# Performance work log

Measured on AMD Instinct MI355X. Metric: run time of the kernel, lower is better.

Reference implementation:

```python
import jax, jax.numpy as jnp
import numpy as np

C = 768            # config.channels
CH, CW = 16, 16    # coarse span shape for group 'screen'
N = CH * CW        # total coarse positions = 256
FH, FW, FP = 16, 16, 2
F = FH * FW * FP   # fine_total = 512
K = 4              # top4 sample mode
B = 1024           # sb


def _ln(x, g, b, eps=1e-5):
    m = jnp.mean(x, axis=-1, keepdims=True)
    v = jnp.mean((x - m) ** 2, axis=-1, keepdims=True)
    return (x - m) / jnp.sqrt(v + eps) * g + b


def _mlp3(x, W1, b1, W2, b2, W3, b3):
    h = jax.nn.gelu(x @ W1 + b1)
    h = jax.nn.gelu(h @ W2 + b2)
    return h @ W3 + b3


def setup_inputs() -> dict:
    key = jax.random.key(0)
    ks = jax.random.split(key, 16)

    def w(k, fan_in, shape):
        return jax.random.normal(k, shape, jnp.float32) * (1.0 / np.sqrt(fan_in))

    return {
        "x": jax.random.normal(ks[0], (B, C), jnp.float32),
        "g_in": jnp.ones((C,), jnp.float32),
        "b_in": jnp.zeros((C,), jnp.float32),
        # coarse head: C -> C -> C -> N
        "cW1": w(ks[1], C, (C, C)), "cb1": jnp.zeros((C,), jnp.float32),
        "cW2": w(ks[2], C, (C, C)), "cb2": jnp.zeros((C,), jnp.float32),
        "cW3": w(ks[3], C, (C, N)), "cb3": jnp.zeros((N,), jnp.float32),
        # coarse embedding
        "emb": jax.random.normal(ks[4], (N, C), jnp.float32),
        "g_e": jnp.ones((C,), jnp.float32),
        "b_e": jnp.zeros((C,), jnp.float32),
        # fine head: 2C -> C -> C -> F
        "fW1": w(ks[5], 2 * C, (2 * C, C)), "fb1": jnp.zeros((C,), jnp.float32),
        "fW2": w(ks[6], C, (C, C)), "fb2": jnp.zeros((C,), jnp.float32),
        "fW3": w(ks[7], C, (C, F)), "fb3": jnp.zeros((F,), jnp.float32),
        # no-op head
        "nW": w(ks[8], C, (C, 1)), "nb": jnp.zeros((1,), jnp.float32),
    }


def reference(x, g_in, b_in, cW1, cb1, cW2, cb2, cW3, cb3, emb, g_e, b_e,
              fW1, fb1, fW2, fb2, fW3, fb3, nW, nb):
    b = x.shape[0]
    xn = _ln(x, g_in, b_in)                                   # (b, C)
    no_op = xn @ nW + nb                                      # (b, 1)
    coarse = _mlp3(xn, cW1, cb1, cW2, cb2, cW3, cb3)          # (b, N)

    # top4 routing
    _, i = jax.lax.top_k(coarse, K)                           # (b, K) int32
    e = _ln(emb[i], g_e, b_e)                                 # (b, K, C)
    fine_in = jnp.concatenate(
        [jnp.broadcast_to(xn[:, None, :], (b, K, C)), e], axis=-1)  # (b, K, 2C)
    fine = _mlp3(fine_in, fW1, fb1, fW2, fb2, fW3, fb3)       # (b, K, F)

    log_f = jnp.log(jnp.float32(F))
    xfull = jnp.broadcast_to(coarse[:, :, None], (b, N, F)) - log_f  # (b, N, F)
    upd = fine + log_f - jax.nn.logsumexp(fine, axis=-1, keepdims=True)
    xfull = xfull.at[jnp.arange(b)[:, None], i].add(upd)      # scatter-combine

    # per-group permute: (b, ch, cw, fh, fw, fp) -> (b, ch, fh, cw, fw, fp)
    xg = xfull.reshape(b, CH, CW, FH, FW, FP)
    xg = jnp.transpose(xg, (0, 1, 3, 2, 4, 5)).reshape(b, -1)
    return jnp.concatenate([no_op, xg], axis=-1)              # (b, 1 + N*F)
```

## Files before the change

### kernel.cpp

```cpp
#include <hip/hip_runtime.h>
#include <hip/hip_bf16.h>
#include <math.h>

typedef unsigned short u16;
typedef unsigned int   u32;
typedef __attribute__((ext_vector_type(8))) short s16x8;
typedef __attribute__((ext_vector_type(4))) float f32x4;

#define CB 768
#define NB 256
#define FB 512
#define BATCH 1024
#define OUTC 131073
#define LOGF 6.2383246250395077f

#define OFF_X    0
#define OFF_GIN  786432
#define OFF_BIN  787200
#define OFF_CW1  787968
#define OFF_CB1  1377792
#define OFF_CW2  1378560
#define OFF_CB2  1968384
#define OFF_CW3  1969152
#define OFF_CB3  2165760
#define OFF_EMB  2166016
#define OFF_GE   2362624
#define OFF_BE   2363392
#define OFF_FW1  2364160
#define OFF_FB1  3543808
#define OFF_FW2  3544576
#define OFF_FB2  4134400
#define OFF_FW3  4135168
#define OFF_FB3  4528384
#define OFF_NW   4528896
#define OFF_NB   4529664
#define MASTER_TOTAL 4529665

struct Ptrs20 { const void* p[20]; };

__device__ __forceinline__ u16 f2bf(float f){
    u32 u = __float_as_uint(f);
    u32 r = u + 0x7FFFu + ((u >> 16) & 1u);
    return (u16)(r >> 16);
}
__device__ __forceinline__ float bf2f(u16 s){ return __uint_as_float(((u32)s) << 16); }

__device__ __forceinline__ float gelu_f(float x){
    return 0.5f * x * (1.0f + tanhf(0.7978845608028654f * (x + 0.044715f * x * x * x)));
}

__device__ __forceinline__ f32x4 mfma16x16x32(s16x8 a, s16x8 b, f32x4 c){
    return __builtin_amdgcn_mfma_f32_16x16x32_bf16(a, b, c, 0, 0, 0);
}

__device__ __forceinline__ float blockReduce(float v, float* sb, bool domax){
    #pragma unroll
    for (int o = 32; o > 0; o >>= 1){
        float ov = __shfl_down(v, o, 64);
        v = domax ? fmaxf(v, ov) : (v + ov);
    }
    int w = threadIdx.x >> 6, lane = threadIdx.x & 63;
    if (lane == 0) sb[w] = v;
    __syncthreads();
    float r = domax ? fmaxf(fmaxf(sb[0], sb[1]), fmaxf(sb[2], sb[3]))
                    : (sb[0] + sb[1] + sb[2] + sb[3]);
    __syncthreads();
    return r;
}

__global__ __launch_bounds__(256) void convert_k(Ptrs20 ip, float* __restrict__ m){
    const int SZ[20]  = {786432,768,768,589824,768,589824,768,196608,256,196608,
                         768,768,1179648,768,589824,768,393216,512,768,1};
    const int OFF[20] = {OFF_X,OFF_GIN,OFF_BIN,OFF_CW1,OFF_CB1,OFF_CW2,OFF_CB2,OFF_CW3,OFF_CB3,OFF_EMB,
                         OFF_GE,OFF_BE,OFF_FW1,OFF_FB1,OFF_FW2,OFF_FB2,OFF_FW3,OFF_FB3,OFF_NW,OFF_NB};
    int t = blockIdx.y;
    int n = SZ[t];
    int i0 = (blockIdx.x * 256 + threadIdx.x) * 4;
    if (i0 >= n) return;
    bool isbf = (((const u16*)ip.p[1])[0] == 0x3F80u);
    float* dst = m + OFF[t] + i0;
    if (isbf){
        const u16* s = (const u16*)ip.p[t] + i0;
        #pragma unroll
        for (int e = 0; e < 4; e++) if (i0 + e < n) dst[e] = bf2f(s[e]);
    } else {
        const float* s = (const float*)ip.p[t] + i0;
        #pragma unroll
        for (int e = 0; e < 4; e++) if (i0 + e < n) dst[e] = s[e];
    }
}

template<int SPL>
__global__ __launch_bounds__(256) void transpose_k(const float* __restrict__ W,
        u16* __restrict__ Wh, u16* __restrict__ Wl, int K, int N){
    __shared__ float t[32][33];
    int n0 = blockIdx.x * 32, k0 = blockIdx.y * 32;
    int tx = threadIdx.x & 31, ty = threadIdx.x >> 5;
    #pragma unroll
    for (int i = 0; i < 32; i += 8)
        t[ty + i][tx] = W[(size_t)(k0 + ty + i) * N + n0 + tx];
    __syncthreads();
    #pragma unroll
    for (int i = 0; i < 32; i += 8){
        float f = t[tx][ty + i];
        u16 h = f2bf(f);
        Wh[(size_t)(n0 + ty + i) * K + k0 + tx] = h;
        if (SPL == 2)
            Wl[(size_t)(n0 + ty + i) * K + k0 + tx] = f2bf(f - bf2f(h));
    }
}

__global__ __launch_bounds__(256) void ln_x_k(const float* __restrict__ x,
        const float* __restrict__ g, const float* __restrict__ bb,
        const float* __restrict__ nW, const float* __restrict__ nb,
        float* __restrict__ xn_f32, u16* __restrict__ xn_bf, float* __restrict__ noop){
    __shared__ float sb[4];
    int b = blockIdx.x, tid = threadIdx.x;
    const float* xr = x + (size_t)b * CB;
    float v[3];
    #pragma unroll
    for (int i = 0; i < 3; i++) v[i] = xr[tid + i * 256];
    float mean = blockReduce(v[0] + v[1] + v[2], sb, false) * (1.0f / 768.0f);
    float d0 = v[0] - mean, d1 = v[1] - mean, d2 = v[2] - mean;
    float var = blockReduce(d0*d0 + d1*d1 + d2*d2, sb, false) * (1.0f / 768.0f);
    float inv = 1.0f / sqrtf(var + 1e-5f);
    float dot = 0.0f;
    #pragma unroll
    for (int i = 0; i < 3; i++){
        int c = tid + i * 256;
        float xi = (v[i] - mean) * inv * g[c] + bb[c];
        xn_f32[(size_t)b * CB + c] = xi;
        xn_bf[(size_t)b * CB + c] = f2bf(xi);
        dot += xi * nW[c];
    }
    dot = blockReduce(dot, sb, false);
    if (tid == 0) noop[b] = dot + nb[0];
}

template<int ASPLIT, int BSPLIT, int ACT, int OUTBF>
__global__ __launch_bounds__(256) void gemm_k(const void* __restrict__ Ap,
        const u16* __restrict__ Bth, const u16* __restrict__ Btl,
        const float* __restrict__ bias, void* __restrict__ Outp, int M, int N, int K){
    constexpr int LDA = 40;
    __shared__ u16 As[ASPLIT][128 * LDA];
    __shared__ u16 Bs[BSPLIT][64 * LDA];
    const int m0 = blockIdx.y * 128, n0 = blockIdx.x * 64;
    const int tid = threadIdx.x;
    const int w = tid >> 6, lane = tid & 63, lm = lane & 15, q = lane >> 4;
    f32x4 acc[2][4];
    #pragma unroll
    for (int i = 0; i < 2; i++)
        #pragma unroll
        for (int j = 0; j < 4; j++) acc[i][j] = (f32x4)(0.0f);
    const int ar = tid >> 1, ac = (tid & 1) * 16;
    const int bn = tid >> 2, bc = (tid & 3) * 8;

    for (int k0 = 0; k0 < K; k0 += 32){
        __syncthreads();
        if (ASPLIT == 3){
            const float* src = (const float*)Ap + (size_t)(m0 + ar) * K + k0 + ac;
            short hi[16], lo[16], l2[16];
            #pragma unroll
            for (int h = 0; h < 4; h++){
                float4 vv = ((const float4*)src)[h];
                float e4[4] = {vv.x, vv.y, vv.z, vv.w};
                #pragma unroll
                for (int e = 0; e < 4; e++){
                    float f = e4[e];
                    u16 hb = f2bf(f);  float fh = bf2f(hb);
                    float r1 = f - fh; u16 lb = f2bf(r1); float fl = bf2f(lb);
                    float r2 = r1 - fl; u16 qb = f2bf(r2);
                    hi[h*4+e] = (short)hb; lo[h*4+e] = (short)lb; l2[h*4+e] = (short)qb;
                }
            }
            *(s16x8*)&As[0][ar*LDA + ac]     = *(s16x8*)&hi[0];
            *(s16x8*)&As[0][ar*LDA + ac + 8] = *(s16x8*)&hi[8];
            *(s16x8*)&As[1][ar*LDA + ac]     = *(s16x8*)&lo[0];
            *(s16x8*)&As[1][ar*LDA + ac + 8] = *(s16x8*)&lo[8];
            *(s16x8*)&As[2][ar*LDA + ac]     = *(s16x8*)&l2[0];
            *(s16x8*)&As[2][ar*LDA + ac + 8] = *(s16x8*)&l2[8];
        } else {
            const u16* src = (const u16*)Ap + (size_t)(m0 + ar) * K + k0 + ac;
            *(s16x8*)&As[0][ar*LDA + ac]     = *(const s16x8*)(src);
            *(s16x8*)&As[0][ar*LDA + ac + 8] = *(const s16x8*)(src + 8);
        }
        *(s16x8*)&Bs[0][bn*LDA + bc] = *(const s16x8*)(Bth + (size_t)(n0 + bn) * K + k0 + bc);
        if (BSPLIT == 2)
            *(s16x8*)&Bs[1][bn*LDA + bc] = *(const s16x8*)(Btl + (size_t)(n0 + bn) * K + k0 + bc);
        __syncthreads();

        s16x8 afr[ASPLIT][2], bfr[BSPLIT][4];
        #pragma unroll
        for (int mt = 0; mt < 2; mt++)
            #pragma unroll
            for (int s = 0; s < ASPLIT; s++)
                afr[s][mt] = *(const s16x8*)&As[s][(w*32 + mt*16 + lm)*LDA + q*8];
        #pragma unroll
        for (int nt = 0; nt < 4; nt++)
            #pragma unroll
            for (int s = 0; s < BSPLIT; s++)
                bfr[s][nt] = *(const s16x8*)&Bs[s][(nt*16 + lm)*LDA + q*8];
        #pragma unroll
        for (int mt = 0; mt < 2; mt++)
            #pragma unroll
            for (int nt = 0; nt < 4; nt++){
                acc[mt][nt] = mfma16x16x32(afr[0][mt], bfr[0][nt], acc[mt][nt]);
                if (ASPLIT == 3){
                    acc[mt][nt] = mfma16x16x32(afr[1][mt], bfr[0][nt], acc[mt][nt]);
                    acc[mt][nt] = mfma16x16x32(afr[2][mt], bfr[0][nt], acc[mt][nt]);
                }
                if (BSPLIT == 2){
                    acc[mt][nt] = mfma16x16x32(afr[0][mt], bfr[1][nt], acc[mt][nt]);
                    if (ASPLIT == 3)
                        acc[mt][nt] = mfma16x16x32(afr[1][mt], bfr[1][nt], acc[mt][nt]);
                }
            }
    }
    #pragma unroll
    for (int nt = 0; nt < 4; nt++){
        int n = n0 + nt*16 + lm;
        float bv = bias[n];
        #pragma unroll
        for (int mt = 0; mt < 2; mt++){
            #pragma unroll
            for (int r = 0; r < 4; r++){
                int m = m0 + w*32 + mt*16 + q*4 + r;
                float vv = acc[mt][nt][r] + bv;
                if (ACT == 1) vv = gelu_f(vv);
                if (OUTBF) ((u16*)Outp)[(size_t)m * N + n] = f2bf(vv);
                else       ((float*)Outp)[(size_t)m * N + n] = vv;
            }
        }
    }
}

__global__ __launch_bounds__(64) void topk_k(const float* __restrict__ coarse,
        int* __restrict__ idx, unsigned char* __restrict__ ksel){
    int b = blockIdx.x, lane = threadIdx.x;
    const float* cr = coarse + (size_t)b * NB;
    float v[4]; int id[4];
    #pragma unroll
    for (int j = 0; j < 4; j++){ id[j] = lane + 64*j; v[j] = cr[id[j]]; }
    ((u32*)(ksel + (size_t)b * NB))[lane] = 0xFFFFFFFFu;
    __syncthreads();
    for (int k = 0; k < 4; k++){
        float bv = v[0]; int bi = id[0];
        #pragma unroll
        for (int j = 1; j < 4; j++)
            if (v[j] > bv || (v[j] == bv && id[j] < bi)){ bv = v[j]; bi = id[j]; }
        #pragma unroll
        for (int o = 32; o > 0; o >>= 1){
            float ov = __shfl_xor(bv, o, 64);
            int   oi = __shfl_xor(bi, o, 64);
            if (ov > bv || (ov == bv && oi < bi)){ bv = ov; bi = oi; }
        }
        if (lane == 0){ idx[b*4 + k] = bi; ksel[(size_t)b * NB + bi] = (unsigned char)k; }
        #pragma unroll
        for (int j = 0; j < 4; j++) if (id[j] == bi) v[j] = -INFINITY;
    }
}

__global__ __launch_bounds__(256) void finein_k(const int* __restrict__ idx,
        const float* __restrict__ emb, const float* __restrict__ ge, const float* __restrict__ be,
        const u16* __restrict__ xnb, u16* __restrict__ fin){
    __shared__ float sb[4];
    int bk = blockIdx.x, tid = threadIdx.x;
    int b = bk >> 2;
    int n = idx[bk];
    const float* er = emb + (size_t)n * CB;
    float v[3];
    #pragma unroll
    for (int i = 0; i < 3; i++) v[i] = er[tid + i * 256];
    float mean = blockReduce(v[0] + v[1] + v[2], sb, false) * (1.0f / 768.0f);
    float d0 = v[0] - mean, d1 = v[1] - mean, d2 = v[2] - mean;
    float var = blockReduce(d0*d0 + d1*d1 + d2*d2, sb, false) * (1.0f / 768.0f);
    float inv = 1.0f / sqrtf(var + 1e-5f);
    u16* dst = fin + (size_t)bk * (2 * CB);
    #pragma unroll
    for (int i = 0; i < 3; i++){
        int c = tid + i * 256;
        dst[c] = xnb[(size_t)b * CB + c];
        dst[CB + c] = f2bf((v[i] - mean) * inv * ge[c] + be[c]);
    }
}

__global__ __launch_bounds__(256) void upd_k(float* __restrict__ fine){
    __shared__ float sb[4];
    int bk = blockIdx.x, tid = threadIdx.x;
    float* fr = fine + (size_t)bk * FB;
    float a = fr[tid], b2 = fr[tid + 256];
    float mx = blockReduce(fmaxf(a, b2), sb, true);
    float es = expf(a - mx) + expf(b2 - mx);
    float ssum = blockReduce(es, sb, false);
    float off = LOGF - (mx + logf(ssum));
    fr[tid] = a + off;
    fr[tid + 256] = b2 + off;
}

__global__ __launch_bounds__(256) void out_k(const float* __restrict__ coarse,
        const float* __restrict__ upd, const unsigned char* __restrict__ ksel,
        const float* __restrict__ noop, const void* __restrict__ g_in_raw,
        void* __restrict__ outp){
    u32 g0 = ((u32)blockIdx.x * 256u + (u32)threadIdx.x) * 8u;
    const u32 total = (u32)BATCH * (u32)OUTC;
    if (g0 >= total) return;
    bool isbf = (((const u16*)g_in_raw)[0] == 0x3F80u);
    float vals[8];
    #pragma unroll
    for (int e = 0; e < 8; e++){
        u32 gg = g0 + (u32)e;
        u32 qq = gg >> 17;
        int rr = (int)(gg & 131071u) - (int)qq;
        if (rr < 0){ qq -= 1u; rr += 131073; }
        int b = (int)qq;
        float val;
        if (rr == 0){
            val = noop[b];
        } else {
            int j = rr - 1;
            int ch = j >> 13;
            int rem = j & 8191;
            int fh = rem >> 9, cw = (rem >> 5) & 15, ff = rem & 31;
            int n = (ch << 4) + cw;
            val = coarse[(size_t)b * NB + n] - LOGF;
            int ks = ksel[(size_t)b * NB + n];
            if (ks != 255) val += upd[(((size_t)b * 4 + ks) << 9) + (fh << 5) + ff];
        }
        vals[e] = val;
    }
    if (isbf){
        u16 res[8];
        #pragma unroll
        for (int e = 0; e < 8; e++) res[e] = f2bf(vals[e]);
        *(s16x8*)((u16*)outp + g0) = *(s16x8*)res;
    } else {
        float* of = (float*)outp + g0;
        *(float4*)(of)     = make_float4(vals[0], vals[1], vals[2], vals[3]);
        *(float4*)(of + 4) = make_float4(vals[4], vals[5], vals[6], vals[7]);
    }
}

extern "C" void kernel_launch(void* const* d_in, const int* in_sizes, int n_in,
                              void* d_out, int out_size, void* d_ws, size_t ws_size,
                              hipStream_t stream){
    (void)in_sizes; (void)n_in; (void)out_size; (void)ws_size;
    char* ws = (char*)d_ws;
    size_t off = 0;
    auto alloc = [&](size_t bytes){ void* p = ws + off; off += (bytes + 255) & ~(size_t)255; return p; };

    float* master = (float*)alloc((size_t)MASTER_TOTAL * 4);
    u16*   xn_bf  = (u16*)  alloc((size_t)1024*768*2);
    u16*   fin    = (u16*)  alloc((size_t)4096*1536*2);
    float* fine   = (float*)alloc((size_t)4096*512*4);
    u16*   gg1    = (u16*)  alloc((size_t)4096*768*2);
    u16*   gg2    = (u16*)  alloc((size_t)4096*768*2);
    float* coarse = (float*)alloc((size_t)1024*256*4);
    int*   idx    = (int*)  alloc((size_t)1024*4*4);
    unsigned char* ksel = (unsigned char*)alloc((size_t)1024*256);
    float* noop   = (float*)alloc((size_t)1024*4);
    u16* cW1th = (u16*)alloc((size_t)768*768*2);
    u16* cW1tl = (u16*)alloc((size_t)768*768*2);
    u16* cW2th = (u16*)alloc((size_t)768*768*2);
    u16* cW2tl = (u16*)alloc((size_t)768*768*2);
    u16* cW3th = (u16*)alloc((size_t)768*256*2);
    u16* cW3tl = (u16*)alloc((size_t)768*256*2);
    u16* fW1t  = (u16*)alloc((size_t)1536*768*2);
    u16* fW2t  = (u16*)alloc((size_t)768*768*2);
    u16* fW3t  = (u16*)alloc((size_t)768*512*2);

    float* xn_f32 = (float*)fin;
    float* h1     = (float*)fine;
    float* h2     = (float*)gg1;

    Ptrs20 ip;
    for (int i = 0; i < 20; i++) ip.p[i] = d_in[i];

    convert_k<<<dim3(1152, 20), 256, 0, stream>>>(ip, master);

    transpose_k<2><<<dim3(24, 24), 256, 0, stream>>>(master + OFF_CW1, cW1th, cW1tl, 768, 768);
    transpose_k<2><<<dim3(24, 24), 256, 0, stream>>>(master + OFF_CW2, cW2th, cW2tl, 768, 768);
    transpose_k<2><<<dim3( 8, 24), 256, 0, stream>>>(master + OFF_CW3, cW3th, cW3tl, 768, 256);
    transpose_k<1><<<dim3(24, 48), 256, 0, stream>>>(master + OFF_FW1, fW1t, nullptr, 1536, 768);
    transpose_k<1><<<dim3(24, 24), 256, 0, stream>>>(master + OFF_FW2, fW2t, nullptr, 768, 768);
    transpose_k<1><<<dim3(16, 24), 256, 0, stream>>>(master + OFF_FW3, fW3t, nullptr, 768, 512);

    ln_x_k<<<1024, 256, 0, stream>>>(master + OFF_X, master + OFF_GIN, master + OFF_BIN,
                                     master + OFF_NW, master + OFF_NB, xn_f32, xn_bf, noop);

    gemm_k<3,2,1,0><<<dim3(12, 8), 256, 0, stream>>>(xn_f32, cW1th, cW1tl, master + OFF_CB1, h1, 1024, 768, 768);
    gemm_k<3,2,1,0><<<dim3(12, 8), 256, 0, stream>>>(h1,     cW2th, cW2tl, master + OFF_CB2, h2, 1024, 768, 768);
    gemm_k<3,2,0,0><<<dim3( 4, 8), 256, 0, stream>>>(h2,     cW3th, cW3tl, master + OFF_CB3, coarse, 1024, 256, 768);

    topk_k<<<1024, 64, 0, stream>>>(coarse, idx, ksel);
    finein_k<<<4096, 256, 0, stream>>>(idx, master + OFF_EMB, master + OFF_GE, master + OFF_BE, xn_bf, fin);

    gemm_k<1,1,1,1><<<dim3(12, 32), 256, 0, stream>>>(fin, fW1t, nullptr, master + OFF_FB1, gg1, 4096, 768, 1536);
    gemm_k<1,1,1,1><<<dim3(12, 32), 256, 0, stream>>>(gg1, fW2t, nullptr, master + OFF_FB2, gg2, 4096, 768, 768);
    gemm_k<1,1,0,0><<<dim3( 8, 32), 256, 0, stream>>>(gg2, fW3t, nullptr, master + OFF_FB3, fine, 4096, 512, 768);

    upd_k<<<4096, 256, 0, stream>>>(fine);

    u32 total_chunks = ((u32)BATCH * (u32)OUTC) / 8u;
    u32 blocks = (total_chunks + 255u) / 256u;
    out_k<<<blocks, 256, 0, stream>>>(coarse, fine, ksel, noop, d_in[1], d_out);
}
```

Baseline: 874.1 us.

## Drop fp32 staging copy, merge transposes, presplit activations, fuse softmax offset into output

Removes the convert kernel that copied all inputs into an fp32 master buffer; kernels now read the raw inputs directly and detect the dtype per load. The six weight transposes are merged into one launch driven by a descriptor table. Coarse-head activations are split into three bf16 parts once, in the producing kernel's epilogue, instead of being re-split inside every GEMM tile load. The in-place logsumexp update pass is replaced by a per-row offset kernel whose offset is added inside the output kernel. This cuts launches and redundant traffic and conversion work, at the cost of more intermediate buffers and three-way stores from the GEMM epilogue.

```diff
diff --git a/kernel.cpp b/kernel.cpp
--- a/kernel.cpp
+++ b/kernel.cpp
@@ -14,41 +14,24 @@
 #define OUTC 131073
 #define LOGF 6.2383246250395077f
 
-#define OFF_X    0
-#define OFF_GIN  786432
-#define OFF_BIN  787200
-#define OFF_CW1  787968
-#define OFF_CB1  1377792
-#define OFF_CW2  1378560
-#define OFF_CB2  1968384
-#define OFF_CW3  1969152
-#define OFF_CB3  2165760
-#define OFF_EMB  2166016
-#define OFF_GE   2362624
-#define OFF_BE   2363392
-#define OFF_FW1  2364160
-#define OFF_FB1  3543808
-#define OFF_FW2  3544576
-#define OFF_FB2  4134400
-#define OFF_FW3  4135168
-#define OFF_FB3  4528384
-#define OFF_NW   4528896
-#define OFF_NB   4529664
-#define MASTER_TOTAL 4529665
-
-struct Ptrs20 { const void* p[20]; };
-
 __device__ __forceinline__ u16 f2bf(float f){
     u32 u = __float_as_uint(f);
     u32 r = u + 0x7FFFu + ((u >> 16) & 1u);
     return (u16)(r >> 16);
 }
 __device__ __forceinline__ float bf2f(u16 s){ return __uint_as_float(((u32)s) << 16); }
-
+__device__ __forceinline__ bool probe_bf(const void* g){ return ((const u16*)g)[0] == 0x3F80u; }
+__device__ __forceinline__ float loadraw(const void* p, size_t i, bool isbf){
+    return isbf ? bf2f(((const u16*)p)[i]) : ((const float*)p)[i];
+}
+__device__ __forceinline__ void split3(float f, u16& h, u16& l, u16& q){
+    h = f2bf(f); float r1 = f - bf2f(h);
+    l = f2bf(r1); float r2 = r1 - bf2f(l);
+    q = f2bf(r2);
+}
 __device__ __forceinline__ float gelu_f(float x){
     return 0.5f * x * (1.0f + tanhf(0.7978845608028654f * (x + 0.044715f * x * x * x)));
 }
-
 __device__ __forceinline__ f32x4 mfma16x16x32(s16x8 a, s16x8 b, f32x4 c){
     return __builtin_amdgcn_mfma_f32_16x16x32_bf16(a, b, c, 0, 0, 0);
 }
@@ -68,58 +51,45 @@
     return r;
 }
 
-__global__ __launch_bounds__(256) void convert_k(Ptrs20 ip, float* __restrict__ m){
-    const int SZ[20]  = {786432,768,768,589824,768,589824,768,196608,256,196608,
-                         768,768,1179648,768,589824,768,393216,512,768,1};
-    const int OFF[20] = {OFF_X,OFF_GIN,OFF_BIN,OFF_CW1,OFF_CB1,OFF_CW2,OFF_CB2,OFF_CW3,OFF_CB3,OFF_EMB,
-                         OFF_GE,OFF_BE,OFF_FW1,OFF_FB1,OFF_FW2,OFF_FB2,OFF_FW3,OFF_FB3,OFF_NW,OFF_NB};
-    int t = blockIdx.y;
-    int n = SZ[t];
-    int i0 = (blockIdx.x * 256 + threadIdx.x) * 4;
-    if (i0 >= n) return;
-    bool isbf = (((const u16*)ip.p[1])[0] == 0x3F80u);
-    float* dst = m + OFF[t] + i0;
-    if (isbf){
-        const u16* s = (const u16*)ip.p[t] + i0;
-        #pragma unroll
-        for (int e = 0; e < 4; e++) if (i0 + e < n) dst[e] = bf2f(s[e]);
-    } else {
-        const float* s = (const float*)ip.p[t] + i0;
-        #pragma unroll
-        for (int e = 0; e < 4; e++) if (i0 + e < n) dst[e] = s[e];
-    }
-}
-
-template<int SPL>
-__global__ __launch_bounds__(256) void transpose_k(const float* __restrict__ W,
-        u16* __restrict__ Wh, u16* __restrict__ Wl, int K, int N){
+struct TransDesc { const void* src; u16* dh; u16* dl; int K; int N; int start; int tilesX; };
+struct TD6 { TransDesc d[6]; };
+
+__global__ __launch_bounds__(256) void transpose_all_k(TD6 td, const void* ginp){
+    bool isbf = probe_bf(ginp);
+    int blk = blockIdx.x;
+    int e = 0;
+    #pragma unroll
+    for (int i = 1; i < 6; i++) if (blk >= td.d[i].start) e = i;
+    TransDesc d = td.d[e];
+    int rel = blk - d.start;
+    int n0 = (rel % d.tilesX) * 32;
+    int k0 = (rel / d.tilesX) * 32;
     __shared__ float t[32][33];
-    int n0 = blockIdx.x * 32, k0 = blockIdx.y * 32;
     int tx = threadIdx.x & 31, ty = threadIdx.x >> 5;
     #pragma unroll
     for (int i = 0; i < 32; i += 8)
-        t[ty + i][tx] = W[(size_t)(k0 + ty + i) * N + n0 + tx];
+        t[ty + i][tx] = loadraw(d.src, (size_t)(k0 + ty + i) * d.N + n0 + tx, isbf);
     __syncthreads();
     #pragma unroll
     for (int i = 0; i < 32; i += 8){
         float f = t[tx][ty + i];
         u16 h = f2bf(f);
-        Wh[(size_t)(n0 + ty + i) * K + k0 + tx] = h;
-        if (SPL == 2)
-            Wl[(size_t)(n0 + ty + i) * K + k0 + tx] = f2bf(f - bf2f(h));
-    }
-}
-
-__global__ __launch_bounds__(256) void ln_x_k(const float* __restrict__ x,
-        const float* __restrict__ g, const float* __restrict__ bb,
-        const float* __restrict__ nW, const float* __restrict__ nb,
-        float* __restrict__ xn_f32, u16* __restrict__ xn_bf, float* __restrict__ noop){
+        d.dh[(size_t)(n0 + ty + i) * d.K + k0 + tx] = h;
+        if (d.dl)
+            d.dl[(size_t)(n0 + ty + i) * d.K + k0 + tx] = f2bf(f - bf2f(h));
+    }
+}
+
+__global__ __launch_bounds__(256) void ln_x_k(const void* x, const void* g, const void* bb,
+        const void* nW, const void* nb, const void* ginp,
+        u16* __restrict__ xh, u16* __restrict__ xl, u16* __restrict__ xq,
+        float* __restrict__ noop){
     __shared__ float sb[4];
+    bool isbf = probe_bf(ginp);
     int b = blockIdx.x, tid = threadIdx.x;
-    const float* xr = x + (size_t)b * CB;
     float v[3];
     #pragma unroll
-    for (int i = 0; i < 3; i++) v[i] = xr[tid + i * 256];
+    for (int i = 0; i < 3; i++) v[i] = loadraw(x, (size_t)b * CB + tid + i * 256, isbf);
     float mean = blockReduce(v[0] + v[1] + v[2], sb, false) * (1.0f / 768.0f);
     float d0 = v[0] - mean, d1 = v[1] - mean, d2 = v[2] - mean;
     float var = blockReduce(d0*d0 + d1*d1 + d2*d2, sb, false) * (1.0f / 768.0f);
@@ -128,22 +98,27 @@
     #pragma unroll
     for (int i = 0; i < 3; i++){
         int c = tid + i * 256;
-        float xi = (v[i] - mean) * inv * g[c] + bb[c];
-        xn_f32[(size_t)b * CB + c] = xi;
-        xn_bf[(size_t)b * CB + c] = f2bf(xi);
-        dot += xi * nW[c];
+        float xi = (v[i] - mean) * inv * loadraw(g, c, isbf) + loadraw(bb, c, isbf);
+        u16 h, l, q; split3(xi, h, l, q);
+        size_t o = (size_t)b * CB + c;
+        xh[o] = h; xl[o] = l; xq[o] = q;
+        dot += xi * loadraw(nW, c, isbf);
     }
     dot = blockReduce(dot, sb, false);
-    if (tid == 0) noop[b] = dot + nb[0];
-}
-
-template<int ASPLIT, int BSPLIT, int ACT, int OUTBF>
-__global__ __launch_bounds__(256) void gemm_k(const void* __restrict__ Ap,
+    if (tid == 0) noop[b] = dot + loadraw(nb, 0, isbf);
+}
+
+template<int ASPLIT, int BSPLIT, int ACT, int OUTMODE>
+__global__ __launch_bounds__(256) void gemm_k(
+        const u16* __restrict__ Ah, const u16* __restrict__ Al, const u16* __restrict__ Aq,
         const u16* __restrict__ Bth, const u16* __restrict__ Btl,
-        const float* __restrict__ bias, void* __restrict__ Outp, int M, int N, int K){
+        const void* __restrict__ bias, const void* __restrict__ ginp,
+        void* __restrict__ o0, void* __restrict__ o1, void* __restrict__ o2,
+        int M, int N, int K){
     constexpr int LDA = 40;
     __shared__ u16 As[ASPLIT][128 * LDA];
     __shared__ u16 Bs[BSPLIT][64 * LDA];
+    bool isbf = probe_bf(ginp);
     const int m0 = blockIdx.y * 128, n0 = blockIdx.x * 64;
     const int tid = threadIdx.x;
     const int w = tid >> 6, lane = tid & 63, lm = lane & 15, q = lane >> 4;
@@ -157,32 +132,18 @@
 
     for (int k0 = 0; k0 < K; k0 += 32){
         __syncthreads();
-        if (ASPLIT == 3){
-            const float* src = (const float*)Ap + (size_t)(m0 + ar) * K + k0 + ac;
-            short hi[16], lo[16], l2[16];
-            #pragma unroll
-            for (int h = 0; h < 4; h++){
-                float4 vv = ((const float4*)src)[h];
-                float e4[4] = {vv.x, vv.y, vv.z, vv.w};
-                #pragma unroll
-                for (int e = 0; e < 4; e++){
-                    float f = e4[e];
-                    u16 hb = f2bf(f);  float fh = bf2f(hb);
-                    float r1 = f - fh; u16 lb = f2bf(r1); float fl = bf2f(lb);
-                    float r2 = r1 - fl; u16 qb = f2bf(r2);
-                    hi[h*4+e] = (short)hb; lo[h*4+e] = (short)lb; l2[h*4+e] = (short)qb;
-                }
+        {
+            const u16* s0 = Ah + (size_t)(m0 + ar) * K + k0 + ac;
+            *(s16x8*)&As[0][ar*LDA + ac]     = *(const s16x8*)(s0);
+            *(s16x8*)&As[0][ar*LDA + ac + 8] = *(const s16x8*)(s0 + 8);
+            if (ASPLIT == 3){
+                const u16* s1 = Al + (size_t)(m0 + ar) * K + k0 + ac;
+                *(s16x8*)&As[1][ar*LDA + ac]     = *(const s16x8*)(s1);
+                *(s16x8*)&As[1][ar*LDA + ac + 8] = *(const s16x8*)(s1 + 8);
+                const u16* s2 = Aq + (size_t)(m0 + ar) * K + k0 + ac;
+                *(s16x8*)&As[2][ar*LDA + ac]     = *(const s16x8*)(s2);
+                *(s16x8*)&As[2][ar*LDA + ac + 8] = *(const s16x8*)(s2 + 8);
             }
-            *(s16x8*)&As[0][ar*LDA + ac]     = *(s16x8*)&hi[0];
-            *(s16x8*)&As[0][ar*LDA + ac + 8] = *(s16x8*)&hi[8];
-            *(s16x8*)&As[1][ar*LDA + ac]     = *(s16x8*)&lo[0];
-            *(s16x8*)&As[1][ar*LDA + ac + 8] = *(s16x8*)&lo[8];
-            *(s16x8*)&As[2][ar*LDA + ac]     = *(s16x8*)&l2[0];
-            *(s16x8*)&As[2][ar*LDA + ac + 8] = *(s16x8*)&l2[8];
-        } else {
-            const u16* src = (const u16*)Ap + (size_t)(m0 + ar) * K + k0 + ac;
-            *(s16x8*)&As[0][ar*LDA + ac]     = *(const s16x8*)(src);
-            *(s16x8*)&As[0][ar*LDA + ac + 8] = *(const s16x8*)(src + 8);
         }
         *(s16x8*)&Bs[0][bn*LDA + bc] = *(const s16x8*)(Bth + (size_t)(n0 + bn) * K + k0 + bc);
         if (BSPLIT == 2)
@@ -219,7 +180,7 @@
     #pragma unroll
     for (int nt = 0; nt < 4; nt++){
         int n = n0 + nt*16 + lm;
-        float bv = bias[n];
+        float bv = loadraw(bias, n, isbf);
         #pragma unroll
         for (int mt = 0; mt < 2; mt++){
             #pragma unroll
@@ -227,8 +188,13 @@
                 int m = m0 + w*32 + mt*16 + q*4 + r;
                 float vv = acc[mt][nt][r] + bv;
                 if (ACT == 1) vv = gelu_f(vv);
-                if (OUTBF) ((u16*)Outp)[(size_t)m * N + n] = f2bf(vv);
-                else       ((float*)Outp)[(size_t)m * N + n] = vv;
+                size_t o = (size_t)m * N + n;
+                if (OUTMODE == 0)      ((float*)o0)[o] = vv;
+                else if (OUTMODE == 1) ((u16*)o0)[o] = f2bf(vv);
+                else {
+                    u16 h, l, qq; split3(vv, h, l, qq);
+                    ((u16*)o0)[o] = h; ((u16*)o1)[o] = l; ((u16*)o2)[o] = qq;
+                }
             }
         }
     }
@@ -261,16 +227,16 @@
 }
 
 __global__ __launch_bounds__(256) void finein_k(const int* __restrict__ idx,
-        const float* __restrict__ emb, const float* __restrict__ ge, const float* __restrict__ be,
-        const u16* __restrict__ xnb, u16* __restrict__ fin){
+        const void* __restrict__ emb, const void* __restrict__ ge, const void* __restrict__ be,
+        const void* __restrict__ ginp, const u16* __restrict__ xh, u16* __restrict__ fin){
     __shared__ float sb[4];
+    bool isbf = probe_bf(ginp);
     int bk = blockIdx.x, tid = threadIdx.x;
     int b = bk >> 2;
     int n = idx[bk];
-    const float* er = emb + (size_t)n * CB;
     float v[3];
     #pragma unroll
-    for (int i = 0; i < 3; i++) v[i] = er[tid + i * 256];
+    for (int i = 0; i < 3; i++) v[i] = loadraw(emb, (size_t)n * CB + tid + i * 256, isbf);
     float mean = blockReduce(v[0] + v[1] + v[2], sb, false) * (1.0f / 768.0f);
     float d0 = v[0] - mean, d1 = v[1] - mean, d2 = v[2] - mean;
     float var = blockReduce(d0*d0 + d1*d1 + d2*d2, sb, false) * (1.0f / 768.0f);
@@ -279,32 +245,40 @@
     #pragma unroll
     for (int i = 0; i < 3; i++){
         int c = tid + i * 256;
-        dst[c] = xnb[(size_t)b * CB + c];
-        dst[CB + c] = f2bf((v[i] - mean) * inv * ge[c] + be[c]);
-    }
-}
-
-__global__ __launch_bounds__(256) void upd_k(float* __restrict__ fine){
-    __shared__ float sb[4];
-    int bk = blockIdx.x, tid = threadIdx.x;
-    float* fr = fine + (size_t)bk * FB;
-    float a = fr[tid], b2 = fr[tid + 256];
-    float mx = blockReduce(fmaxf(a, b2), sb, true);
-    float es = expf(a - mx) + expf(b2 - mx);
-    float ssum = blockReduce(es, sb, false);
-    float off = LOGF - (mx + logf(ssum));
-    fr[tid] = a + off;
-    fr[tid + 256] = b2 + off;
+        dst[c] = xh[(size_t)b * CB + c];
+        dst[CB + c] = f2bf((v[i] - mean) * inv * loadraw(ge, c, isbf) + loadraw(be, c, isbf));
+    }
+}
+
+__global__ __launch_bounds__(256) void updoff_k(const float* __restrict__ fine,
+        float* __restrict__ offs){
+    int row = blockIdx.x * 4 + (threadIdx.x >> 6);
+    int lane = threadIdx.x & 63;
+    const float* fr = fine + (size_t)row * FB;
+    float v[8];
+    #pragma unroll
+    for (int j = 0; j < 8; j++) v[j] = fr[lane + 64*j];
+    float mx = v[0];
+    #pragma unroll
+    for (int j = 1; j < 8; j++) mx = fmaxf(mx, v[j]);
+    #pragma unroll
+    for (int o = 32; o > 0; o >>= 1) mx = fmaxf(mx, __shfl_xor(mx, o, 64));
+    float es = 0.0f;
+    #pragma unroll
+    for (int j = 0; j < 8; j++) es += expf(v[j] - mx);
+    #pragma unroll
+    for (int o = 32; o > 0; o >>= 1) es += __shfl_xor(es, o, 64);
+    if (lane == 0) offs[row] = LOGF - (mx + logf(es));
 }
 
 __global__ __launch_bounds__(256) void out_k(const float* __restrict__ coarse,
-        const float* __restrict__ upd, const unsigned char* __restrict__ ksel,
-        const float* __restrict__ noop, const void* __restrict__ g_in_raw,
-        void* __restrict__ outp){
+        const float* __restrict__ fine, const float* __restrict__ offs,
+        const unsigned char* __restrict__ ksel, const float* __restrict__ noop,
+        const void* __restrict__ ginp, void* __restrict__ outp){
     u32 g0 = ((u32)blockIdx.x * 256u + (u32)threadIdx.x) * 8u;
     const u32 total = (u32)BATCH * (u32)OUTC;
     if (g0 >= total) return;
-    bool isbf = (((const u16*)g_in_raw)[0] == 0x3F80u);
+    bool isbf = probe_bf(ginp);
     float vals[8];
     #pragma unroll
     for (int e = 0; e < 8; e++){
@@ -324,7 +298,10 @@
             int n = (ch << 4) + cw;
             val = coarse[(size_t)b * NB + n] - LOGF;
             int ks = ksel[(size_t)b * NB + n];
-            if (ks != 255) val += upd[(((size_t)b * 4 + ks) << 9) + (fh << 5) + ff];
+            if (ks != 255){
+                int fr = b * 4 + ks;
+                val += fine[((size_t)fr << 9) + (fh << 5) + ff] + offs[fr];
+            }
         }
         vals[e] = val;
     }
@@ -348,16 +325,24 @@
     size_t off = 0;
     auto alloc = [&](size_t bytes){ void* p = ws + off; off += (bytes + 255) & ~(size_t)255; return p; };
 
-    float* master = (float*)alloc((size_t)MASTER_TOTAL * 4);
-    u16*   xn_bf  = (u16*)  alloc((size_t)1024*768*2);
-    u16*   fin    = (u16*)  alloc((size_t)4096*1536*2);
-    float* fine   = (float*)alloc((size_t)4096*512*4);
-    u16*   gg1    = (u16*)  alloc((size_t)4096*768*2);
-    u16*   gg2    = (u16*)  alloc((size_t)4096*768*2);
+    u16* xh  = (u16*)alloc((size_t)1024*768*2);
+    u16* xl  = (u16*)alloc((size_t)1024*768*2);
+    u16* xq  = (u16*)alloc((size_t)1024*768*2);
+    u16* h1h = (u16*)alloc((size_t)1024*768*2);
+    u16* h1l = (u16*)alloc((size_t)1024*768*2);
+    u16* h1q = (u16*)alloc((size_t)1024*768*2);
+    u16* h2h = (u16*)alloc((size_t)1024*768*2);
+    u16* h2l = (u16*)alloc((size_t)1024*768*2);
+    u16* h2q = (u16*)alloc((size_t)1024*768*2);
     float* coarse = (float*)alloc((size_t)1024*256*4);
     int*   idx    = (int*)  alloc((size_t)1024*4*4);
     unsigned char* ksel = (unsigned char*)alloc((size_t)1024*256);
     float* noop   = (float*)alloc((size_t)1024*4);
+    float* offs   = (float*)alloc((size_t)4096*4);
+    u16*   fin    = (u16*)  alloc((size_t)4096*1536*2);
+    u16*   gg1    = (u16*)  alloc((size_t)4096*768*2);
+    u16*   gg2    = (u16*)  alloc((size_t)4096*768*2);
+    float* fine   = (float*)alloc((size_t)4096*512*4);
     u16* cW1th = (u16*)alloc((size_t)768*768*2);
     u16* cW1tl = (u16*)alloc((size_t)768*768*2);
     u16* cW2th = (u16*)alloc((size_t)768*768*2);
@@ -368,39 +353,40 @@
     u16* fW2t  = (u16*)alloc((size_t)768*768*2);
     u16* fW3t  = (u16*)alloc((size_t)768*512*2);
 
-    float* xn_f32 = (float*)fin;
-    float* h1     = (float*)fine;
-    float* h2     = (float*)gg1;
-
-    Ptrs20 ip;
-    for (int i = 0; i < 20; i++) ip.p[i] = d_in[i];
-
-    convert_k<<<dim3(1152, 20), 256, 0, stream>>>(ip, master);
-
-    transpose_k<2><<<dim3(24, 24), 256, 0, stream>>>(master + OFF_CW1, cW1th, cW1tl, 768, 768);
-    transpose_k<2><<<dim3(24, 24), 256, 0, stream>>>(master + OFF_CW2, cW2th, cW2tl, 768, 768);
-    transpose_k<2><<<dim3( 8, 24), 256, 0, stream>>>(master + OFF_CW3, cW3th, cW3tl, 768, 256);
-    transpose_k<1><<<dim3(24, 48), 256, 0, stream>>>(master + OFF_FW1, fW1t, nullptr, 1536, 768);
-    transpose_k<1><<<dim3(24, 24), 256, 0, stream>>>(master + OFF_FW2, fW2t, nullptr, 768, 768);
-    transpose_k<1><<<dim3(16, 24), 256, 0, stream>>>(master + OFF_FW3, fW3t, nullptr, 768, 512);
-
-    ln_x_k<<<1024, 256, 0, stream>>>(master + OFF_X, master + OFF_GIN, master + OFF_BIN,
-                                     master + OFF_NW, master + OFF_NB, xn_f32, xn_bf, noop);
-
-    gemm_k<3,2,1,0><<<dim3(12, 8), 256, 0, stream>>>(xn_f32, cW1th, cW1tl, master + OFF_CB1, h1, 1024, 768, 768);
-    gemm_k<3,2,1,0><<<dim3(12, 8), 256, 0, stream>>>(h1,     cW2th, cW2tl, master + OFF_CB2, h2, 1024, 768, 768);
-    gemm_k<3,2,0,0><<<dim3( 4, 8), 256, 0, stream>>>(h2,     cW3th, cW3tl, master + OFF_CB3, coarse, 1024, 256, 768);
+    const void* ginp = d_in[1];
+
+    TD6 td;
+    td.d[0] = { d_in[3],  cW1th, cW1tl,  768, 768,    0, 24 };
+    td.d[1] = { d_in[5],  cW2th, cW2tl,  768, 768,  576, 24 };
+    td.d[2] = { d_in[7],  cW3th, cW3tl,  768, 256, 1152,  8 };
+    td.d[3] = { d_in[12], fW1t,  nullptr,1536, 768, 1344, 24 };
+    td.d[4] = { d_in[14], fW2t,  nullptr, 768, 768, 2496, 24 };
+    td.d[5] = { d_in[16], fW3t,  nullptr, 768, 512, 3072, 16 };
+    transpose_all_k<<<3456, 256, 0, stream>>>(td, ginp);
+
+    ln_x_k<<<1024, 256, 0, stream>>>(d_in[0], d_in[1], d_in[2], d_in[18], d_in[19],
+                                     ginp, xh, xl, xq, noop);
+
+    gemm_k<3,2,1,2><<<dim3(12, 8), 256, 0, stream>>>(xh, xl, xq, cW1th, cW1tl,
+            d_in[4], ginp, h1h, h1l, h1q, 1024, 768, 768);
+    gemm_k<3,2,1,2><<<dim3(12, 8), 256, 0, stream>>>(h1h, h1l, h1q, cW2th, cW2tl,
+            d_in[6], ginp, h2h, h2l, h2q, 1024, 768, 768);
+    gemm_k<3,2,0,0><<<dim3( 4, 8), 256, 0, stream>>>(h2h, h2l, h2q, cW3th, cW3tl,
+            d_in[8], ginp, coarse, nullptr, nullptr, 1024, 256, 768);
 
     topk_k<<<1024, 64, 0, stream>>>(coarse, idx, ksel);
-    finein_k<<<4096, 256, 0, stream>>>(idx, master + OFF_EMB, master + OFF_GE, master + OFF_BE, xn_bf, fin);
-
-    gemm_k<1,1,1,1><<<dim3(12, 32), 256, 0, stream>>>(fin, fW1t, nullptr, master + OFF_FB1, gg1, 4096, 768, 1536);
-    gemm_k<1,1,1,1><<<dim3(12, 32), 256, 0, stream>>>(gg1, fW2t, nullptr, master + OFF_FB2, gg2, 4096, 768, 768);
-    gemm_k<1,1,0,0><<<dim3( 8, 32), 256, 0, stream>>>(gg2, fW3t, nullptr, master + OFF_FB3, fine, 4096, 512, 768);
-
-    upd_k<<<4096, 256, 0, stream>>>(fine);
+    finein_k<<<4096, 256, 0, stream>>>(idx, d_in[9], d_in[10], d_in[11], ginp, xh, fin);
+
+    gemm_k<1,1,1,1><<<dim3(12, 32), 256, 0, stream>>>(fin, nullptr, nullptr, fW1t, nullptr,
+            d_in[13], ginp, gg1, nullptr, nullptr, 4096, 768, 1536);
+    gemm_k<1,1,1,1><<<dim3(12, 32), 256, 0, stream>>>(gg1, nullptr, nullptr, fW2t, nullptr,
+            d_in[15], ginp, gg2, nullptr, nullptr, 4096, 768, 768);
+    gemm_k<1,1,0,0><<<dim3( 8, 32), 256, 0, stream>>>(gg2, nullptr, nullptr, fW3t, nullptr,
+            d_in[17], ginp, fine, nullptr, nullptr, 4096, 512, 768);
+
+    updoff_k<<<1024, 256, 0, stream>>>(fine, offs);
 
     u32 total_chunks = ((u32)BATCH * (u32)OUTC) / 8u;
     u32 blocks = (total_chunks + 255u) / 256u;
-    out_k<<<blocks, 256, 0, stream>>>(coarse, fine, ksel, noop, d_in[1], d_out);
-}
+    out_k<<<blocks, 256, 0, stream>>>(coarse, fine, offs, ksel, noop, ginp, d_out);
+}
```

After: 840.1 us. -3.9%, faster.
